# Performance work log

Hardware: AMD Instinct MI355X
Metric: run time of the kernel (lower is better)

The kernel has to match this reference:

```python
import jax, jax.numpy as jnp
import numpy as np

DIM = 768
HEADS = 12
DH = DIM // HEADS
SCALE = DH ** -0.5


def setup_inputs() -> dict:
    key = jax.random.key(0)
    ks = jax.random.split(key, 8)
    B, N = 8, 1024
    x = jax.random.normal(ks[0], (B, N, DIM), dtype=jnp.float32)
    rpb = jax.random.normal(ks[1], (1, HEADS, N, N), dtype=jnp.float32)
    s = DIM ** -0.5
    W_qkv = jax.random.normal(ks[2], (DIM, 3 * DIM), dtype=jnp.float32) * s
    W_out = jax.random.normal(ks[3], (DIM, DIM), dtype=jnp.float32) * s
    b_out = jnp.zeros((DIM,), dtype=jnp.float32)
    ln_g = jnp.ones((DIM,), dtype=jnp.float32)
    ln_b = jnp.zeros((DIM,), dtype=jnp.float32)
    return {"x": x, "relative_position_bias": rpb, "W_qkv": W_qkv,
            "W_out": W_out, "b_out": b_out, "ln_g": ln_g, "ln_b": ln_b}


def reference(x, relative_position_bias, W_qkv, W_out, b_out, ln_g, ln_b):
    # LayerNorm (eps matches torch default 1e-5)
    mu = jnp.mean(x, axis=-1, keepdims=True)
    var = jnp.mean(jnp.square(x - mu), axis=-1, keepdims=True)
    xn = (x - mu) * jax.lax.rsqrt(var + 1e-5) * ln_g + ln_b

    qkv = xn @ W_qkv                                  # [b,n,3*dim]
    q, k, v = jnp.split(qkv, 3, axis=-1)
    B, N, _ = x.shape
    reshape = lambda t: t.reshape(B, N, HEADS, DH).transpose(0, 2, 1, 3)  # b h n d
    q, k, v = reshape(q), reshape(k), reshape(v)

    scores = jnp.einsum('bhid,bhjd->bhij', q, k) * SCALE + relative_position_bias
    attn = jax.nn.softmax(scores, axis=-1)            # dropout p=0.0 -> identity
    out = jnp.einsum('bhij,bhjd->bhid', attn, v)
    out = out.transpose(0, 2, 1, 3).reshape(B, N, HEADS * DH)
    return out @ W_out + b_out
```

## Files before the change

kernel.cpp:

```cpp
#include <hip/hip_runtime.h>
#include <hip/hip_bf16.h>
#include <math.h>

#define BATCH 8
#define NSEQ  1024
#define DIMM  768
#define NHEAD 12
#define DHEAD 64
#define SCALE 0.125f
#define ROWS  (BATCH * NSEQ)

typedef __hip_bfloat16 bf16;
typedef __bf16 bf16x8 __attribute__((ext_vector_type(8)));
typedef float  f32x4  __attribute__((ext_vector_type(4)));

#if __has_builtin(__builtin_amdgcn_global_load_lds)
#define HAVE_GLL 1
typedef __attribute__((address_space(3))) void lds_void_t;
typedef const __attribute__((address_space(1))) void gbl_void_t;
__device__ __forceinline__ void gload16(const void* g, void* l) {
    __builtin_amdgcn_global_load_lds((gbl_void_t*)g, (lds_void_t*)l, 16, 0, 0);
}
#else
#define HAVE_GLL 0
#endif

__device__ __forceinline__ unsigned pk2(float a, float b) {
    union { unsigned u; bf16 h[2]; } x;
    x.h[0] = __float2bfloat16(a);
    x.h[1] = __float2bfloat16(b);
    return x.u;
}

__global__ __launch_bounds__(256) void ln_kernel(const float* __restrict__ x,
                                                 const float* __restrict__ g,
                                                 const float* __restrict__ bta,
                                                 bf16* __restrict__ y) {
    __shared__ float ps[4], pq[4];
    __shared__ float mean_s, rstd_s;
    int row = blockIdx.x;
    int tid = threadIdx.x;
    const float* xr = x + (size_t)row * DIMM;
    float v[3];
    float s = 0.f, sq = 0.f;
#pragma unroll
    for (int i = 0; i < 3; ++i) {
        v[i] = xr[tid + 256 * i];
        s += v[i];
        sq += v[i] * v[i];
    }
#pragma unroll
    for (int off = 32; off >= 1; off >>= 1) {
        s  += __shfl_down(s, off);
        sq += __shfl_down(sq, off);
    }
    int wid = tid >> 6, lane = tid & 63;
    if (lane == 0) { ps[wid] = s; pq[wid] = sq; }
    __syncthreads();
    if (tid == 0) {
        float S = ps[0] + ps[1] + ps[2] + ps[3];
        float Q = pq[0] + pq[1] + pq[2] + pq[3];
        float mean = S * (1.0f / DIMM);
        float var  = Q * (1.0f / DIMM) - mean * mean;
        mean_s = mean;
        rstd_s = rsqrtf(fmaxf(var, 0.f) + 1e-5f);
    }
    __syncthreads();
    float mean = mean_s, rstd = rstd_s;
    bf16* yr = y + (size_t)row * DIMM;
#pragma unroll
    for (int i = 0; i < 3; ++i) {
        int c = tid + 256 * i;
        yr[c] = __float2bfloat16((v[i] - mean) * rstd * g[c] + bta[c]);
    }
}

__global__ __launch_bounds__(256) void transpose_bf16(const float* __restrict__ W,
                                                      bf16* __restrict__ Wt,
                                                      int K, int N) {
    __shared__ float t[32][33];
    int n0 = blockIdx.x * 32, k0 = blockIdx.y * 32;
    int tx = threadIdx.x, ty = threadIdx.y;
#pragma unroll
    for (int i = 0; i < 32; i += 8)
        t[ty + i][tx] = W[(size_t)(k0 + ty + i) * N + n0 + tx];
    __syncthreads();
#pragma unroll
    for (int i = 0; i < 32; i += 8)
        Wt[(size_t)(n0 + ty + i) * K + k0 + tx] = __float2bfloat16(t[tx][ty + i]);
}

template <bool OUT_BF16>
__global__ __launch_bounds__(256) void gemm_mfma(const bf16* __restrict__ A,
                                                 const bf16* __restrict__ Bt,
                                                 const float* __restrict__ bias,
                                                 void* __restrict__ Cv,
                                                 int M, int Nn, int K) {
    __shared__ bf16 As[128][32];
    __shared__ bf16 Bs[128][32];
    int tid = threadIdx.x;
    int wave = tid >> 6, lane = tid & 63, quad = lane >> 4, l16 = lane & 15;
    int wm = (wave >> 1) * 64, wn = (wave & 1) * 64;
    int m0 = blockIdx.y * 128, n0 = blockIdx.x * 128;

    f32x4 acc[4][4] = {};

#if HAVE_GLL
    const char* Ag = (const char*)(A  + (size_t)(m0 + (tid >> 2)) * K + (tid & 3) * 8);
    const char* Bg = (const char*)(Bt + (size_t)(n0 + (tid >> 2)) * K + (tid & 3) * 8);
    char* AsB = (char*)&As[0][0] + tid * 16;
    char* BsB = (char*)&Bs[0][0] + tid * 16;
    const size_t radv = (size_t)64 * K * 2;

    for (int k0 = 0; k0 < K; k0 += 32) {
        __syncthreads();
        gload16(Ag, AsB);
        gload16(Ag + radv, AsB + 4096);
        gload16(Bg, BsB);
        gload16(Bg + radv, BsB + 4096);
        Ag += 64; Bg += 64;
        __syncthreads();
#else
    int srow = tid >> 1;
    int sk = (tid & 1) * 16;
    const bf16* Ap = A  + (size_t)(m0 + srow) * K + sk;
    const bf16* Bp = Bt + (size_t)(n0 + srow) * K + sk;
    for (int k0 = 0; k0 < K; k0 += 32) {
        uint4 a0 = *(const uint4*)(Ap + k0);
        uint4 a1 = *(const uint4*)(Ap + k0 + 8);
        uint4 b0 = *(const uint4*)(Bp + k0);
        uint4 b1 = *(const uint4*)(Bp + k0 + 8);
        __syncthreads();
        *(uint4*)&As[srow][sk]     = a0;
        *(uint4*)&As[srow][sk + 8] = a1;
        *(uint4*)&Bs[srow][sk]     = b0;
        *(uint4*)&Bs[srow][sk + 8] = b1;
        __syncthreads();
#endif
        bf16x8 af[4], bf_[4];
#pragma unroll
        for (int i = 0; i < 4; ++i) {
            af[i]  = *(const bf16x8*)&As[wm + i * 16 + l16][quad * 8];
            bf_[i] = *(const bf16x8*)&Bs[wn + i * 16 + l16][quad * 8];
        }
#pragma unroll
        for (int mi = 0; mi < 4; ++mi)
#pragma unroll
            for (int ni = 0; ni < 4; ++ni)
                acc[mi][ni] = __builtin_amdgcn_mfma_f32_16x16x32_bf16(
                    af[mi], bf_[ni], acc[mi][ni], 0, 0, 0);
    }

    float bv[4] = {0.f, 0.f, 0.f, 0.f};
    if (!OUT_BF16 && bias) {
#pragma unroll
        for (int ni = 0; ni < 4; ++ni) bv[ni] = bias[n0 + wn + ni * 16 + l16];
    }
#pragma unroll
    for (int mi = 0; mi < 4; ++mi)
#pragma unroll
        for (int reg = 0; reg < 4; ++reg) {
            size_t row = m0 + wm + mi * 16 + quad * 4 + reg;
#pragma unroll
            for (int ni = 0; ni < 4; ++ni) {
                int col = n0 + wn + ni * 16 + l16;
                float val = acc[mi][ni][reg] + bv[ni];
                if (OUT_BF16)
                    ((bf16*)Cv)[row * Nn + col] = __float2bfloat16(val);
                else
                    ((float*)Cv)[row * Nn + col] = val;
            }
        }
}

#define KTILEB (64 * 3 * DIMM * 2)
#define NBLK   (BATCH * NHEAD * (NSEQ / 64))

__global__ __launch_bounds__(256, 4) void attn_mfma(const bf16* __restrict__ qkv,
                                                    const float* __restrict__ rpb,
                                                    bf16* __restrict__ outb) {
    __shared__ char KsRaw[2][8192];
    __shared__ unsigned Vt32[2][64][36];
    __shared__ bf16 Ps[4][16][72];

    int tid = threadIdx.x;
    int wave = tid >> 6, lane = tid & 63, quad = lane >> 4, l16 = lane & 15;

    int p   = blockIdx.x;
    int wid = (p & 7) * (NBLK / 8) + (p >> 3);
    int h   = wid >> 7;
    int rem = wid & 127;
    int b   = rem >> 4;
    int mt  = rem & 15;
    int m0  = mt * 64;

    const bf16* qrow = qkv + (size_t)(b * NSEQ + m0 + wave * 16 + l16) * (3 * DIMM) + h * DHEAD;
    bf16x8 qf0 = *(const bf16x8*)(qrow + quad * 8);
    bf16x8 qf1 = *(const bf16x8*)(qrow + 32 + quad * 8);

    const float* rp = rpb + ((size_t)h * NSEQ + (m0 + wave * 16 + l16)) * NSEQ;

#if HAVE_GLL
    const char* kgl = (const char*)(qkv + (size_t)(b * NSEQ + wave * 16 + l16) * (3 * DIMM)
                                    + DIMM + h * DHEAD + quad * 8);
    char* kdst = &KsRaw[0][0] + tid * 16 + wave * 1024;
#else
    int ksr = tid >> 2, ksd = (tid & 3) * 16;
    const bf16* kgf = qkv + (size_t)(b * NSEQ + ksr) * (3 * DIMM) + DIMM + h * DHEAD + ksd;
#endif

    int vk = (tid >> 3) * 2;
    int vd = (tid & 7) * 8;
    int vkp = tid >> 3;
    const bf16* vg = qkv + (size_t)(b * NSEQ + vk) * (3 * DIMM) + 2 * DIMM + h * DHEAD + vd;
    int wblk = (((vkp >> 2) ^ (vd >> 3)) << 2) | (vkp & 3);

    float m_s = -INFINITY, l_s = 0.f;
    f32x4 acco[4] = {};

#if HAVE_GLL
    gload16(kgl, kdst);
    gload16(kgl + 64, kdst + 1024);
#endif
    uint4 va = *(const uint4*)(vg);
    uint4 vb = *(const uint4*)(vg + 3 * DIMM);
#if !HAVE_GLL
    {
        uint4 k0v = *(const uint4*)(kgf);
        uint4 k1v = *(const uint4*)(kgf + 8);
        char* d0 = &KsRaw[0][0] + (ksr >> 4) * 2048 + (ksd >> 5) * 1024 + ((((ksd >> 3) & 3) * 16 + (ksr & 15)) * 16);
        *(uint4*)d0 = k0v;
        char* d1 = &KsRaw[0][0] + (ksr >> 4) * 2048 + ((ksd + 8) >> 5) * 1024 + (((((ksd + 8) >> 3) & 3) * 16 + (ksr & 15)) * 16);
        *(uint4*)d1 = k1v;
    }
#endif
    {
        union { uint4 q; unsigned short u[8]; } A_, B_;
        A_.q = va; B_.q = vb;
#pragma unroll
        for (int j = 0; j < 8; ++j)
            Vt32[0][vd + j][wblk] = (unsigned)A_.u[j] | ((unsigned)B_.u[j] << 16);
    }
    float4 rv[4];
#pragma unroll
    for (int t = 0; t < 4; ++t)
        rv[t] = *(const float4*)&rp[t * 16 + quad * 4];
    __syncthreads();

    for (int kt = 0; kt < 16; ++kt) {
        int cur = kt & 1, nxt = cur ^ 1;

        float4 rvn[4];
        if (kt + 1 < 16) {
#if HAVE_GLL
            const char* kg2 = kgl + (size_t)(kt + 1) * KTILEB;
            gload16(kg2, kdst + nxt * 8192);
            gload16(kg2 + 64, kdst + nxt * 8192 + 1024);
#endif
            const bf16* v2 = vg + (size_t)(kt + 1) * 64 * (3 * DIMM);
            va = *(const uint4*)(v2);
            vb = *(const uint4*)(v2 + 3 * DIMM);
            const float* rpn = rp + (kt + 1) * 64;
#pragma unroll
            for (int t = 0; t < 4; ++t)
                rvn[t] = *(const float4*)&rpn[t * 16 + quad * 4];
        }

        f32x4 accs[4] = {};
        __builtin_amdgcn_s_setprio(1);
#pragma unroll
        for (int t = 0; t < 4; ++t) {
            const char* kb = &KsRaw[cur][0] + t * 2048 + (quad * 16 + l16) * 16;
            bf16x8 kf0 = *(const bf16x8*)(kb);
            bf16x8 kf1 = *(const bf16x8*)(kb + 1024);
            accs[t] = __builtin_amdgcn_mfma_f32_16x16x32_bf16(kf0, qf0, accs[t], 0, 0, 0);
            accs[t] = __builtin_amdgcn_mfma_f32_16x16x32_bf16(kf1, qf1, accs[t], 0, 0, 0);
        }
        __builtin_amdgcn_s_setprio(0);

        float mx = -INFINITY;
        {
            float rb[4][4] = {{rv[0].x, rv[0].y, rv[0].z, rv[0].w},
                              {rv[1].x, rv[1].y, rv[1].z, rv[1].w},
                              {rv[2].x, rv[2].y, rv[2].z, rv[2].w},
                              {rv[3].x, rv[3].y, rv[3].z, rv[3].w}};
#pragma unroll
            for (int t = 0; t < 4; ++t)
#pragma unroll
                for (int r = 0; r < 4; ++r) {
                    accs[t][r] = fmaf(accs[t][r], SCALE, rb[t][r]);
                    mx = fmaxf(mx, accs[t][r]);
                }
        }
        mx = fmaxf(mx, __shfl_xor(mx, 16));
        mx = fmaxf(mx, __shfl_xor(mx, 32));
        float mn = fmaxf(m_s, mx);
        float alpha = __expf(m_s - mn);
        m_s = mn;
        float sum = 0.f;
#pragma unroll
        for (int t = 0; t < 4; ++t)
#pragma unroll
            for (int r = 0; r < 4; ++r) {
                float pv = __expf(accs[t][r] - mn);
                accs[t][r] = pv;
                sum += pv;
            }
        sum += __shfl_xor(sum, 16);
        sum += __shfl_xor(sum, 32);
        l_s = l_s * alpha + sum;

        float ab[4];
#pragma unroll
        for (int r = 0; r < 4; ++r) ab[r] = __shfl(alpha, quad * 4 + r);
#pragma unroll
        for (int dt = 0; dt < 4; ++dt)
#pragma unroll
            for (int r = 0; r < 4; ++r) acco[dt][r] *= ab[r];

#pragma unroll
        for (int t = 0; t < 4; ++t) {
            uint2 w;
            w.x = pk2(accs[t][0], accs[t][1]);
            w.y = pk2(accs[t][2], accs[t][3]);
            *(uint2*)&Ps[wave][l16][t * 16 + quad * 4] = w;
        }
        __asm__ volatile("s_waitcnt lgkmcnt(0)" ::: "memory");

        __builtin_amdgcn_s_setprio(1);
#pragma unroll
        for (int s = 0; s < 2; ++s) {
            bf16x8 pf = *(const bf16x8*)&Ps[wave][l16][s * 32 + quad * 8];
#pragma unroll
            for (int dt = 0; dt < 4; ++dt) {
                int row = dt * 16 + l16;
                int sblk = (((s * 4 + quad) ^ ((row >> 3) & 7)) << 2);
                bf16x8 vf = *(const bf16x8*)&Vt32[cur][row][sblk];
                acco[dt] = __builtin_amdgcn_mfma_f32_16x16x32_bf16(pf, vf, acco[dt], 0, 0, 0);
            }
        }
        __builtin_amdgcn_s_setprio(0);

        if (kt + 1 < 16) {
            union { uint4 q; unsigned short u[8]; } A_, B_;
            A_.q = va; B_.q = vb;
#pragma unroll
            for (int j = 0; j < 8; ++j)
                Vt32[nxt][vd + j][wblk] = (unsigned)A_.u[j] | ((unsigned)B_.u[j] << 16);
#pragma unroll
            for (int t = 0; t < 4; ++t) rv[t] = rvn[t];
        }
        __syncthreads();
    }

    float invl[4];
#pragma unroll
    for (int r = 0; r < 4; ++r) invl[r] = 1.f / __shfl(l_s, quad * 4 + r);
    bf16* orow = outb + (size_t)(b * NSEQ + m0 + wave * 16) * DIMM + h * DHEAD;
#pragma unroll
    for (int dt = 0; dt < 4; ++dt)
#pragma unroll
        for (int r = 0; r < 4; ++r)
            orow[(size_t)(quad * 4 + r) * DIMM + dt * 16 + l16] =
                __float2bfloat16(acco[dt][r] * invl[r]);
}

extern "C" void kernel_launch(void* const* d_in, const int* in_sizes, int n_in,
                              void* d_out, int out_size, void* d_ws, size_t ws_size,
                              hipStream_t stream) {
    const float* x     = (const float*)d_in[0];
    const float* rpb   = (const float*)d_in[1];
    const float* W_qkv = (const float*)d_in[2];
    const float* W_out = (const float*)d_in[3];
    const float* b_out = (const float*)d_in[4];
    const float* ln_g  = (const float*)d_in[5];
    const float* ln_b  = (const float*)d_in[6];
    float* out = (float*)d_out;

    char* p = (char*)d_ws;
    bf16* xn    = (bf16*)p; p += (size_t)ROWS * DIMM * 2;
    bf16* qkv   = (bf16*)p; p += (size_t)ROWS * 3 * DIMM * 2;
    bf16* attn  = (bf16*)p; p += (size_t)ROWS * DIMM * 2;
    bf16* WqkvT = (bf16*)p; p += (size_t)3 * DIMM * DIMM * 2;
    bf16* WoutT = (bf16*)p; p += (size_t)DIMM * DIMM * 2;

    ln_kernel<<<ROWS, 256, 0, stream>>>(x, ln_g, ln_b, xn);
    transpose_bf16<<<dim3(3 * DIMM / 32, DIMM / 32), dim3(32, 8), 0, stream>>>(
        W_qkv, WqkvT, DIMM, 3 * DIMM);
    transpose_bf16<<<dim3(DIMM / 32, DIMM / 32), dim3(32, 8), 0, stream>>>(
        W_out, WoutT, DIMM, DIMM);

    gemm_mfma<true><<<dim3(3 * DIMM / 128, ROWS / 128), 256, 0, stream>>>(
        xn, WqkvT, nullptr, qkv, ROWS, 3 * DIMM, DIMM);

    attn_mfma<<<NBLK, 256, 0, stream>>>(qkv, rpb, attn);

    gemm_mfma<false><<<dim3(DIMM / 128, ROWS / 128), 256, 0, stream>>>(
        attn, WoutT, b_out, out, ROWS, DIMM, DIMM);
}
```

Measured before the change: 276.6 us.

## Double-buffer GEMM LDS tiles and add lazy softmax rescaling in attention

The bf16 MFMA GEMM now keeps two LDS buffers for A and B and issues the next k-tile's loads before computing on the current one. This cuts the barriers per iteration from two to one and overlaps global loads with MFMA work, at the cost of twice the shared memory per block. In the flash-attention loop, the running max and the accumulator rescale are now updated only when some lane's new max exceeds the old one by more than 8. This skips the exp, shuffles and multiplies on most tiles but allows exponentials up to e^8 before renormalising.

```diff
diff --git a/kernel.cpp b/kernel.cpp
--- a/kernel.cpp
+++ b/kernel.cpp
@@ -96,8 +96,8 @@
                                                  const float* __restrict__ bias,
                                                  void* __restrict__ Cv,
                                                  int M, int Nn, int K) {
-    __shared__ bf16 As[128][32];
-    __shared__ bf16 Bs[128][32];
+    __shared__ bf16 As[2][128][32];
+    __shared__ bf16 Bs[2][128][32];
     int tid = threadIdx.x;
     int wave = tid >> 6, lane = tid & 63, quad = lane >> 4, l16 = lane & 15;
     int wm = (wave >> 1) * 64, wn = (wave & 1) * 64;
@@ -108,40 +108,59 @@
 #if HAVE_GLL
     const char* Ag = (const char*)(A  + (size_t)(m0 + (tid >> 2)) * K + (tid & 3) * 8);
     const char* Bg = (const char*)(Bt + (size_t)(n0 + (tid >> 2)) * K + (tid & 3) * 8);
-    char* AsB = (char*)&As[0][0] + tid * 16;
-    char* BsB = (char*)&Bs[0][0] + tid * 16;
+    char* AsB = (char*)&As[0][0][0] + tid * 16;
+    char* BsB = (char*)&Bs[0][0][0] + tid * 16;
     const size_t radv = (size_t)64 * K * 2;
 
+    gload16(Ag, AsB);
+    gload16(Ag + radv, AsB + 4096);
+    gload16(Bg, BsB);
+    gload16(Bg + radv, BsB + 4096);
+    Ag += 64; Bg += 64;
+    __syncthreads();
+
+    int cur = 0;
     for (int k0 = 0; k0 < K; k0 += 32) {
-        __syncthreads();
-        gload16(Ag, AsB);
-        gload16(Ag + radv, AsB + 4096);
-        gload16(Bg, BsB);
-        gload16(Bg + radv, BsB + 4096);
-        Ag += 64; Bg += 64;
-        __syncthreads();
+        int nxt = cur ^ 1;
+        if (k0 + 32 < K) {
+            gload16(Ag, AsB + nxt * 8192);
+            gload16(Ag + radv, AsB + nxt * 8192 + 4096);
+            gload16(Bg, BsB + nxt * 8192);
+            gload16(Bg + radv, BsB + nxt * 8192 + 4096);
+            Ag += 64; Bg += 64;
+        }
 #else
     int srow = tid >> 1;
     int sk = (tid & 1) * 16;
     const bf16* Ap = A  + (size_t)(m0 + srow) * K + sk;
     const bf16* Bp = Bt + (size_t)(n0 + srow) * K + sk;
+    {
+        uint4 a0 = *(const uint4*)(Ap);
+        uint4 a1 = *(const uint4*)(Ap + 8);
+        uint4 b0 = *(const uint4*)(Bp);
+        uint4 b1 = *(const uint4*)(Bp + 8);
+        *(uint4*)&As[0][srow][sk]     = a0;
+        *(uint4*)&As[0][srow][sk + 8] = a1;
+        *(uint4*)&Bs[0][srow][sk]     = b0;
+        *(uint4*)&Bs[0][srow][sk + 8] = b1;
+    }
+    __syncthreads();
+    int cur = 0;
     for (int k0 = 0; k0 < K; k0 += 32) {
-        uint4 a0 = *(const uint4*)(Ap + k0);
-        uint4 a1 = *(const uint4*)(Ap + k0 + 8);
-        uint4 b0 = *(const uint4*)(Bp + k0);
-        uint4 b1 = *(const uint4*)(Bp + k0 + 8);
-        __syncthreads();
-        *(uint4*)&As[srow][sk]     = a0;
-        *(uint4*)&As[srow][sk + 8] = a1;
-        *(uint4*)&Bs[srow][sk]     = b0;
-        *(uint4*)&Bs[srow][sk + 8] = b1;
-        __syncthreads();
+        int nxt = cur ^ 1;
+        uint4 a0, a1, b0, b1;
+        if (k0 + 32 < K) {
+            a0 = *(const uint4*)(Ap + k0 + 32);
+            a1 = *(const uint4*)(Ap + k0 + 40);
+            b0 = *(const uint4*)(Bp + k0 + 32);
+            b1 = *(const uint4*)(Bp + k0 + 40);
+        }
 #endif
         bf16x8 af[4], bf_[4];
 #pragma unroll
         for (int i = 0; i < 4; ++i) {
-            af[i]  = *(const bf16x8*)&As[wm + i * 16 + l16][quad * 8];
-            bf_[i] = *(const bf16x8*)&Bs[wn + i * 16 + l16][quad * 8];
+            af[i]  = *(const bf16x8*)&As[cur][wm + i * 16 + l16][quad * 8];
+            bf_[i] = *(const bf16x8*)&Bs[cur][wn + i * 16 + l16][quad * 8];
         }
 #pragma unroll
         for (int mi = 0; mi < 4; ++mi)
@@ -149,6 +168,16 @@
             for (int ni = 0; ni < 4; ++ni)
                 acc[mi][ni] = __builtin_amdgcn_mfma_f32_16x16x32_bf16(
                     af[mi], bf_[ni], acc[mi][ni], 0, 0, 0);
+#if !HAVE_GLL
+        if (k0 + 32 < K) {
+            *(uint4*)&As[nxt][srow][sk]     = a0;
+            *(uint4*)&As[nxt][srow][sk + 8] = a1;
+            *(uint4*)&Bs[nxt][srow][sk]     = b0;
+            *(uint4*)&Bs[nxt][srow][sk + 8] = b1;
+        }
+#endif
+        __syncthreads();
+        cur = nxt;
     }
 
     float bv[4] = {0.f, 0.f, 0.f, 0.f};
@@ -294,29 +323,33 @@
         }
         mx = fmaxf(mx, __shfl_xor(mx, 16));
         mx = fmaxf(mx, __shfl_xor(mx, 32));
-        float mn = fmaxf(m_s, mx);
-        float alpha = __expf(m_s - mn);
-        m_s = mn;
+
+        if (__any(mx > m_s + 8.0f)) {
+            float mn = fmaxf(m_s, mx);
+            float alpha = __expf(m_s - mn);
+            m_s = mn;
+            l_s *= alpha;
+            float ab[4];
+#pragma unroll
+            for (int r = 0; r < 4; ++r) ab[r] = __shfl(alpha, quad * 4 + r);
+#pragma unroll
+            for (int dt = 0; dt < 4; ++dt)
+#pragma unroll
+                for (int r = 0; r < 4; ++r) acco[dt][r] *= ab[r];
+        }
+
         float sum = 0.f;
 #pragma unroll
         for (int t = 0; t < 4; ++t)
 #pragma unroll
             for (int r = 0; r < 4; ++r) {
-                float pv = __expf(accs[t][r] - mn);
+                float pv = __expf(accs[t][r] - m_s);
                 accs[t][r] = pv;
                 sum += pv;
             }
         sum += __shfl_xor(sum, 16);
         sum += __shfl_xor(sum, 32);
-        l_s = l_s * alpha + sum;
-
-        float ab[4];
-#pragma unroll
-        for (int r = 0; r < 4; ++r) ab[r] = __shfl(alpha, quad * 4 + r);
-#pragma unroll
-        for (int dt = 0; dt < 4; ++dt)
-#pragma unroll
-            for (int r = 0; r < 4; ++r) acco[dt][r] *= ab[r];
+        l_s += sum;
 
 #pragma unroll
         for (int t = 0; t < 4; ++t) {
```

After: 270.9 us. 2.1% less time.
